# Kernel optimization log

Measured on AMD Instinct MI355X. Metric: run time of the kernel, lower is better.

Reference implementation:

```python
import jax, jax.numpy as jnp
import numpy as np

HIDDEN_DIM = 1024
BLOCK = 8
NUM_BLOCKS = HIDDEN_DIM // BLOCK


def setup_inputs() -> dict:
    key = jax.random.key(0)
    k1, k2, k3, k4 = jax.random.split(key, 4)
    B, S, D = 4, 4096, HIDDEN_DIM
    return {
        "x_real": jax.random.normal(k1, (B, S, D), dtype=jnp.float32),
        "x_imag": jax.random.normal(k2, (B, S, D), dtype=jnp.float32),
        "A_real": jax.random.normal(k3, (NUM_BLOCKS, BLOCK, BLOCK), dtype=jnp.float32) * 0.02,
        "A_imag": jax.random.normal(k4, (NUM_BLOCKS, BLOCK, BLOCK), dtype=jnp.float32) * 0.02,
    }


def _cayley_unitary(A_real, A_imag):
    # Enforce anti-Hermitian generator: A_r skew-symmetric, A_i symmetric.
    A_r = (A_real - jnp.swapaxes(A_real, -2, -1)) * 0.5
    A_i = (A_imag + jnp.swapaxes(A_imag, -2, -1)) * 0.5
    eye = jnp.eye(BLOCK, dtype=A_real.dtype)[None]  # [1, B, B]
    IpA_r = eye + A_r
    ImA_r = eye - A_r
    # Real-block isomorphism of complex system (I+A) U = (I-A)
    LHS = jnp.concatenate([
        jnp.concatenate([IpA_r, -A_i], axis=-1),
        jnp.concatenate([A_i, IpA_r], axis=-1),
    ], axis=-2)  # [N, 2B, 2B]
    RHS = jnp.concatenate([
        jnp.concatenate([ImA_r, A_i], axis=-1),
        jnp.concatenate([-A_i, ImA_r], axis=-1),
    ], axis=-2)  # [N, 2B, 2B]
    U_rb = jnp.linalg.solve(LHS, RHS)
    return U_rb[:, :BLOCK, :BLOCK], U_rb[:, BLOCK:, :BLOCK]  # (U_real, U_imag)


def reference(x_real, x_imag, A_real, A_imag):
    B, S, D = x_real.shape
    U_real, U_imag = _cayley_unitary(A_real, A_imag)  # each [N, Bk, Bk]
    xr = x_real.reshape(B, S, NUM_BLOCKS, BLOCK)
    xi = x_imag.reshape(B, S, NUM_BLOCKS, BLOCK)
    # Block-diagonal complex matmul: out = U @ x per block
    out_r = jnp.einsum('noi,bsni->bsno', U_real, xr) - jnp.einsum('noi,bsni->bsno', U_imag, xi)
    out_i = jnp.einsum('noi,bsni->bsno', U_real, xi) + jnp.einsum('noi,bsni->bsno', U_imag, xr)
    # Stack real/imag parts of the complex output: [2, B, S, D]
    return jnp.stack([out_r.reshape(B, S, D), out_i.reshape(B, S, D)])
```

## Files before the change

kernel.cpp:

```cpp
#include <hip/hip_runtime.h>

#define NBLK 128
#define BLK  8
#define BB   4
#define SS   4096
#define DD   1024
#define PLANE (BB * SS * DD)
#define APPLY_WGS 1024
#define THREADS (APPLY_WGS * 256)
#define NITER (PLANE / 4 / THREADS)

typedef float floatx4 __attribute__((ext_vector_type(4)));

__global__ __launch_bounds__(64) void cayley_kernel(
    const float* __restrict__ Ar, const float* __restrict__ Ai,
    float* __restrict__ Ur, float* __restrict__ Ui) {
  __shared__ float piv[4][33];
  const int s = threadIdx.x >> 4;
  const int r = threadIdx.x & 15;
  const int n = blockIdx.x * 4 + s;
  const float* arb = Ar + n * 64;
  const float* aib = Ai + n * 64;

  float row[32];
  if (r < 8) {
    #pragma unroll
    for (int c = 0; c < 8; ++c) {
      float sk = 0.5f * (arb[r * 8 + c] - arb[c * 8 + r]);
      float sy = 0.5f * (aib[r * 8 + c] + aib[c * 8 + r]);
      float d  = (c == r) ? 1.0f : 0.0f;
      row[c]      = d + sk;
      row[8 + c]  = -sy;
      row[16 + c] = d - sk;
      row[24 + c] = sy;
    }
  } else {
    const int rr = r - 8;
    #pragma unroll
    for (int c = 0; c < 8; ++c) {
      float sk = 0.5f * (arb[rr * 8 + c] - arb[c * 8 + rr]);
      float sy = 0.5f * (aib[rr * 8 + c] + aib[c * 8 + rr]);
      float d  = (c == rr) ? 1.0f : 0.0f;
      row[c]      = sy;
      row[8 + c]  = d + sk;
      row[16 + c] = -sy;
      row[24 + c] = d - sk;
    }
  }

  #pragma unroll
  for (int k = 0; k < 16; ++k) {
    if (r == k) {
      float inv = 1.0f / row[k];
      #pragma unroll
      for (int j = 0; j < 32; ++j) { row[j] *= inv; piv[s][j] = row[j]; }
    }
    __syncthreads();
    if (r != k) {
      float f = row[k];
      #pragma unroll
      for (int j = 0; j < 32; ++j) row[j] = fmaf(-f, piv[s][j], row[j]);
    }
    __syncthreads();
  }

  if (r < 8) {
    #pragma unroll
    for (int c = 0; c < 8; ++c) Ur[n * 64 + r * 8 + c] = row[16 + c];
  } else {
    #pragma unroll
    for (int c = 0; c < 8; ++c) Ui[n * 64 + (r - 8) * 8 + c] = row[16 + c];
  }
}

__global__ __launch_bounds__(256, 4) void apply_kernel(
    const float* __restrict__ xr, const float* __restrict__ xi,
    const float* __restrict__ Urg, const float* __restrict__ Uig,
    float* __restrict__ out) {
  const int G = blockIdx.x * 256 + threadIdx.x;
  const int p = G & 255;
  const int n = p >> 1;
  const int h = p & 1;

  float u[4][8], v[4][8];
  #pragma unroll
  for (int j = 0; j < 4; ++j) {
    const float* urow = Urg + n * 64 + (h * 4 + j) * 8;
    const float* vrow = Uig + n * 64 + (h * 4 + j) * 8;
    float4 uo = *(const float4*)(urow + h * 4);
    float4 up = *(const float4*)(urow + (h ^ 1) * 4);
    float4 vo = *(const float4*)(vrow + h * 4);
    float4 vp = *(const float4*)(vrow + (h ^ 1) * 4);
    u[j][0] = uo.x; u[j][1] = uo.y; u[j][2] = uo.z; u[j][3] = uo.w;
    u[j][4] = up.x; u[j][5] = up.y; u[j][6] = up.z; u[j][7] = up.w;
    v[j][0] = vo.x; v[j][1] = vo.y; v[j][2] = vo.z; v[j][3] = vo.w;
    v[j][4] = vp.x; v[j][5] = vp.y; v[j][6] = vp.z; v[j][7] = vp.w;
  }
  #pragma unroll
  for (int j = 0; j < 4; ++j)
    #pragma unroll
    for (int c = 0; c < 8; ++c)
      asm volatile("" : "+v"(u[j][c]), "+v"(v[j][c]));

  const float4* pxr = (const float4*)xr;
  const float4* pxi = (const float4*)xi;
  floatx4* qor = (floatx4*)out;
  floatx4* qoi = (floatx4*)(out + PLANE);

  #pragma unroll 2
  for (int k = 0; k < NITER; ++k) {
    const int idx = k * THREADS + G;
    float4 a  = pxr[idx];
    float4 ap = pxr[idx ^ 1];
    float4 b  = pxi[idx];
    float4 bp = pxi[idx ^ 1];

    float oxr[4] = {a.x, a.y, a.z, a.w};
    float oxi[4] = {b.x, b.y, b.z, b.w};
    float wxr[4] = {ap.x, ap.y, ap.z, ap.w};
    float wxi[4] = {bp.x, bp.y, bp.z, bp.w};

    floatx4 sr, si;
    #pragma unroll
    for (int j = 0; j < 4; ++j) {
      float r0 = u[j][0] * oxr[0];
      float i0 = u[j][0] * oxi[0];
      #pragma unroll
      for (int c = 1; c < 4; ++c) {
        r0 = fmaf(u[j][c], oxr[c], r0);
        i0 = fmaf(u[j][c], oxi[c], i0);
      }
      #pragma unroll
      for (int c = 0; c < 4; ++c) {
        r0 = fmaf(u[j][4 + c], wxr[c], r0);
        i0 = fmaf(u[j][4 + c], wxi[c], i0);
      }
      #pragma unroll
      for (int c = 0; c < 4; ++c) {
        r0 = fmaf(-v[j][c], oxi[c], r0);
        i0 = fmaf(v[j][c], oxr[c], i0);
      }
      #pragma unroll
      for (int c = 0; c < 4; ++c) {
        r0 = fmaf(-v[j][4 + c], wxi[c], r0);
        i0 = fmaf(v[j][4 + c], wxr[c], i0);
      }
      sr[j] = r0;
      si[j] = i0;
    }

    asm volatile("global_store_dwordx4 %0, %1, off sc0 sc1 nt"
                 :: "v"(qor + idx), "v"(sr) : "memory");
    asm volatile("global_store_dwordx4 %0, %1, off sc0 sc1 nt"
                 :: "v"(qoi + idx), "v"(si) : "memory");
  }

  asm volatile("s_waitcnt vmcnt(0)" ::: "memory");
}

extern "C" void kernel_launch(void* const* d_in, const int* in_sizes, int n_in,
                              void* d_out, int out_size, void* d_ws, size_t ws_size,
                              hipStream_t stream) {
  const float* xr = (const float*)d_in[0];
  const float* xi = (const float*)d_in[1];
  const float* Ar = (const float*)d_in[2];
  const float* Ai = (const float*)d_in[3];
  float* out = (float*)d_out;

  float* Ur = (float*)d_ws;
  float* Ui = Ur + NBLK * 64;

  cayley_kernel<<<32, 64, 0, stream>>>(Ar, Ai, Ur, Ui);
  apply_kernel<<<APPLY_WGS, 256, 0, stream>>>(xr, xi, Ur, Ui, out);
}
```

Before: 58.29 us.

## Stage inputs into LDS with direct global-to-LDS loads in a 4-deep pipeline

The apply loop is fully unrolled into 16 templated stages. Each stage first issues buffered global_load_lds transfers three chunks ahead into a per-wave 4-slot LDS ring, then waits with explicit vmcnt counts. It reads its own and its neighbour's float4 from LDS instead of issuing two redundant global loads per plane. The aim is to keep more memory requests in flight and remove the duplicate neighbour loads. The cost is 32KB of LDS per block, which may limit occupancy, and hand-tuned waitcnt values that depend on exact instruction ordering.

```diff
diff --git a/kernel.cpp b/kernel.cpp
--- a/kernel.cpp
+++ b/kernel.cpp
@@ -1,7 +1,6 @@
 #include <hip/hip_runtime.h>
 
 #define NBLK 128
-#define BLK  8
 #define BB   4
 #define SS   4096
 #define DD   1024
@@ -73,14 +72,88 @@
   }
 }
 
+__device__ __forceinline__ void stage_chunk(const float4* pxr, const float4* pxi,
+                                            float* slot, int idx) {
+  __builtin_amdgcn_global_load_lds(
+      (const __attribute__((address_space(1))) void*)(pxr + idx),
+      (__attribute__((address_space(3))) void*)slot, 16, 0, 0);
+  __builtin_amdgcn_global_load_lds(
+      (const __attribute__((address_space(1))) void*)(pxi + idx),
+      (__attribute__((address_space(3))) void*)(slot + 256), 16, 0, 0);
+}
+
+template<int K, int W>
+__device__ __forceinline__ void body(const float4* pxr, const float4* pxi,
+                                     floatx4* qor, floatx4* qoi,
+                                     float (*ldsw)[2][256],
+                                     int lane, int G,
+                                     const float (&u)[4][8], const float (&v)[4][8]) {
+  if constexpr (K + 3 < NITER) {
+    stage_chunk(pxr, pxi, &ldsw[(K + 3) & 3][0][0], (K + 3) * THREADS + G);
+  }
+  asm volatile("s_waitcnt vmcnt(%c0)" :: "i"(W) : "memory");
+  __builtin_amdgcn_sched_barrier(0);
+
+  const float* s0 = &ldsw[K & 3][0][0];
+  float4 a  = *(const float4*)(s0 + lane * 4);
+  float4 ap = *(const float4*)(s0 + (lane ^ 1) * 4);
+  float4 b  = *(const float4*)(s0 + 256 + lane * 4);
+  float4 bp = *(const float4*)(s0 + 256 + (lane ^ 1) * 4);
+
+  float oxr[4] = {a.x, a.y, a.z, a.w};
+  float oxi[4] = {b.x, b.y, b.z, b.w};
+  float wxr[4] = {ap.x, ap.y, ap.z, ap.w};
+  float wxi[4] = {bp.x, bp.y, bp.z, bp.w};
+
+  floatx4 sr, si;
+  #pragma unroll
+  for (int j = 0; j < 4; ++j) {
+    float r0 = u[j][0] * oxr[0];
+    float i0 = u[j][0] * oxi[0];
+    #pragma unroll
+    for (int c = 1; c < 4; ++c) {
+      r0 = fmaf(u[j][c], oxr[c], r0);
+      i0 = fmaf(u[j][c], oxi[c], i0);
+    }
+    #pragma unroll
+    for (int c = 0; c < 4; ++c) {
+      r0 = fmaf(u[j][4 + c], wxr[c], r0);
+      i0 = fmaf(u[j][4 + c], wxi[c], i0);
+    }
+    #pragma unroll
+    for (int c = 0; c < 4; ++c) {
+      r0 = fmaf(-v[j][c], oxi[c], r0);
+      i0 = fmaf(v[j][c], oxr[c], i0);
+    }
+    #pragma unroll
+    for (int c = 0; c < 4; ++c) {
+      r0 = fmaf(-v[j][4 + c], wxi[c], r0);
+      i0 = fmaf(v[j][4 + c], wxr[c], i0);
+    }
+    sr[j] = r0;
+    si[j] = i0;
+  }
+
+  const int idx = K * THREADS + G;
+  asm volatile("global_store_dwordx4 %0, %1, off sc0 sc1 nt"
+               :: "v"(qor + idx), "v"(sr) : "memory");
+  asm volatile("global_store_dwordx4 %0, %1, off sc0 sc1 nt"
+               :: "v"(qoi + idx), "v"(si) : "memory");
+}
+
 __global__ __launch_bounds__(256, 4) void apply_kernel(
     const float* __restrict__ xr, const float* __restrict__ xi,
     const float* __restrict__ Urg, const float* __restrict__ Uig,
     float* __restrict__ out) {
-  const int G = blockIdx.x * 256 + threadIdx.x;
+  const int tid  = threadIdx.x;
+  const int wid  = tid >> 6;
+  const int lane = tid & 63;
+  const int G = blockIdx.x * 256 + tid;
   const int p = G & 255;
   const int n = p >> 1;
   const int h = p & 1;
+
+  __shared__ float lds[4][4][2][256];
 
   float u[4][8], v[4][8];
   #pragma unroll
@@ -107,53 +180,28 @@
   floatx4* qor = (floatx4*)out;
   floatx4* qoi = (floatx4*)(out + PLANE);
 
-  #pragma unroll 2
-  for (int k = 0; k < NITER; ++k) {
-    const int idx = k * THREADS + G;
-    float4 a  = pxr[idx];
-    float4 ap = pxr[idx ^ 1];
-    float4 b  = pxi[idx];
-    float4 bp = pxi[idx ^ 1];
-
-    float oxr[4] = {a.x, a.y, a.z, a.w};
-    float oxi[4] = {b.x, b.y, b.z, b.w};
-    float wxr[4] = {ap.x, ap.y, ap.z, ap.w};
-    float wxi[4] = {bp.x, bp.y, bp.z, bp.w};
-
-    floatx4 sr, si;
-    #pragma unroll
-    for (int j = 0; j < 4; ++j) {
-      float r0 = u[j][0] * oxr[0];
-      float i0 = u[j][0] * oxi[0];
-      #pragma unroll
-      for (int c = 1; c < 4; ++c) {
-        r0 = fmaf(u[j][c], oxr[c], r0);
-        i0 = fmaf(u[j][c], oxi[c], i0);
-      }
-      #pragma unroll
-      for (int c = 0; c < 4; ++c) {
-        r0 = fmaf(u[j][4 + c], wxr[c], r0);
-        i0 = fmaf(u[j][4 + c], wxi[c], i0);
-      }
-      #pragma unroll
-      for (int c = 0; c < 4; ++c) {
-        r0 = fmaf(-v[j][c], oxi[c], r0);
-        i0 = fmaf(v[j][c], oxr[c], i0);
-      }
-      #pragma unroll
-      for (int c = 0; c < 4; ++c) {
-        r0 = fmaf(-v[j][4 + c], wxi[c], r0);
-        i0 = fmaf(v[j][4 + c], wxr[c], i0);
-      }
-      sr[j] = r0;
-      si[j] = i0;
-    }
-
-    asm volatile("global_store_dwordx4 %0, %1, off sc0 sc1 nt"
-                 :: "v"(qor + idx), "v"(sr) : "memory");
-    asm volatile("global_store_dwordx4 %0, %1, off sc0 sc1 nt"
-                 :: "v"(qoi + idx), "v"(si) : "memory");
-  }
+  float (*ldsw)[2][256] = lds[wid];
+
+  stage_chunk(pxr, pxi, &ldsw[0][0][0], 0 * THREADS + G);
+  stage_chunk(pxr, pxi, &ldsw[1][0][0], 1 * THREADS + G);
+  stage_chunk(pxr, pxi, &ldsw[2][0][0], 2 * THREADS + G);
+
+  body< 0,  6>(pxr, pxi, qor, qoi, ldsw, lane, G, u, v);
+  body< 1,  8>(pxr, pxi, qor, qoi, ldsw, lane, G, u, v);
+  body< 2, 10>(pxr, pxi, qor, qoi, ldsw, lane, G, u, v);
+  body< 3, 12>(pxr, pxi, qor, qoi, ldsw, lane, G, u, v);
+  body< 4, 12>(pxr, pxi, qor, qoi, ldsw, lane, G, u, v);
+  body< 5, 12>(pxr, pxi, qor, qoi, ldsw, lane, G, u, v);
+  body< 6, 12>(pxr, pxi, qor, qoi, ldsw, lane, G, u, v);
+  body< 7, 12>(pxr, pxi, qor, qoi, ldsw, lane, G, u, v);
+  body< 8, 12>(pxr, pxi, qor, qoi, ldsw, lane, G, u, v);
+  body< 9, 12>(pxr, pxi, qor, qoi, ldsw, lane, G, u, v);
+  body<10, 12>(pxr, pxi, qor, qoi, ldsw, lane, G, u, v);
+  body<11, 12>(pxr, pxi, qor, qoi, ldsw, lane, G, u, v);
+  body<12, 12>(pxr, pxi, qor, qoi, ldsw, lane, G, u, v);
+  body<13, 10>(pxr, pxi, qor, qoi, ldsw, lane, G, u, v);
+  body<14,  8>(pxr, pxi, qor, qoi, ldsw, lane, G, u, v);
+  body<15,  6>(pxr, pxi, qor, qoi, ldsw, lane, G, u, v);
 
   asm volatile("s_waitcnt vmcnt(0)" ::: "memory");
 }
```

Result: slower. 88.86 us (+52.4%).
